# Performance work log

Hardware: AMD Instinct MI355X
Metric: run time of the kernel (lower is better)

## Reference

```python
import jax, jax.numpy as jnp
import numpy as np
import math

DIM = 2048
N_PHASES = 8
B, L = 4, 4096


def setup_inputs() -> dict:
    key = jax.random.key(0)
    ks = jax.random.split(key, 12)
    s = 0.02
    return {
        "x": jax.random.normal(ks[0], (B, L, DIM), dtype=jnp.float32),
        # weights stored [in, out] (transposed vs torch Linear)
        "Wp": jax.random.normal(ks[1], (DIM, N_PHASES), dtype=jnp.float32) * s,
        "bp": jnp.zeros((N_PHASES,), dtype=jnp.float32),
        "Wa": jax.random.normal(ks[2], (DIM, N_PHASES), dtype=jnp.float32) * s,
        "ba": jnp.zeros((N_PHASES,), dtype=jnp.float32),
        "Wv": jax.random.normal(ks[3], (DIM, DIM), dtype=jnp.float32) * s,
        "bv": jnp.zeros((DIM,), dtype=jnp.float32),
        "ln_g": jnp.ones((DIM,), dtype=jnp.float32),
        "ln_b": jnp.zeros((DIM,), dtype=jnp.float32),
        "Wo": jax.random.normal(ks[4], (DIM, DIM), dtype=jnp.float32) * s,
        "bo": jnp.zeros((DIM,), dtype=jnp.float32),
    }


def _layernorm(h, g, b, eps=1e-5):
    mu = jnp.mean(h, axis=-1, keepdims=True)
    var = jnp.var(h, axis=-1, keepdims=True)
    return (h - mu) * jax.lax.rsqrt(var + eps) * g + b


def reference(x, Wp, bp, Wa, ba, Wv, bv, ln_g, ln_b, Wo, bo):
    Llen = x.shape[1]
    phase = jnp.tanh(x @ Wp + bp) * math.pi          # [B,L,P]
    amp = jax.nn.softplus(x @ Wa + ba) + 0.1         # [B,L,P]
    value = x @ Wv + bv                              # [B,L,D]
    # (value[...,None,:] * cos_p[...,None] * amp[...,None]).sum(-2)
    # == value * sum_p(cos_p * amp)  -- algebraic factorization, same math.
    cr = jnp.sum(jnp.cos(phase) * amp, axis=-1, keepdims=True)  # [B,L,1]
    ci = jnp.sum(jnp.sin(phase) * amp, axis=-1, keepdims=True)  # [B,L,1]
    bound = value * (cr + ci)                        # real+imag combined
    retrieved = jnp.cumsum(bound, axis=1)            # [B,L,D]
    h = _layernorm(retrieved / math.sqrt(Llen), ln_g, ln_b)
    return x + h @ Wo + bo
```

## Files before the change

### kernel.cpp

```cpp
#include <hip/hip_runtime.h>

#define DIM   2048
#define LSEQ  4096
#define BATCH 4
#define NTOK  (BATCH*LSEQ)
#define NCH   16
#define CHL   (LSEQ/NCH)
#define PI_F  3.14159265358979f
#define NT    (DIM/64)

typedef __bf16 bf16x8 __attribute__((ext_vector_type(8)));
typedef float  f32x4  __attribute__((ext_vector_type(4)));
typedef float  f32x8  __attribute__((ext_vector_type(8)));
typedef unsigned short ushort4_t __attribute__((ext_vector_type(4)));
typedef unsigned short ushort8 __attribute__((ext_vector_type(8)));

__device__ __forceinline__ unsigned short f2bf(float f) {
    unsigned int u = __float_as_uint(f);
    u += 0x7fffu + ((u >> 16) & 1u);
    return (unsigned short)(u >> 16);
}
__device__ __forceinline__ float bf2f(unsigned short u) {
    return __uint_as_float((unsigned int)u << 16);
}

__device__ __forceinline__ void gload_lds16(const void* g, void* l) {
    __builtin_amdgcn_global_load_lds(
        (const __attribute__((address_space(1))) void*)g,
        (__attribute__((address_space(3))) void*)l, 16, 0, 0);
}

__global__ __launch_bounds__(256) void k_transpose(const float* __restrict__ src,
                                                   unsigned short* __restrict__ dst) {
    __shared__ float tile[32][33];
    int tx = threadIdx.x, ty = threadIdx.y;
    int k0 = blockIdx.y * 32, n0 = blockIdx.x * 32;
#pragma unroll
    for (int r = 0; r < 4; r++)
        tile[ty + r * 8][tx] = src[(size_t)(k0 + ty + r * 8) * DIM + n0 + tx];
    __syncthreads();
#pragma unroll
    for (int r = 0; r < 4; r++)
        dst[(size_t)(n0 + ty + r * 8) * DIM + k0 + tx] = f2bf(tile[tx][ty + r * 8]);
}

__global__ __launch_bounds__(256) void k_prep_wpa(const float* __restrict__ Wp,
                                                  const float* __restrict__ Wa,
                                                  unsigned short* __restrict__ WpaT) {
    int idx = blockIdx.x * 256 + threadIdx.x;
    int p = idx >> 11, k = idx & (DIM - 1);
    float v = (p < 8) ? Wp[(size_t)k * 8 + p] : Wa[(size_t)k * 8 + (p - 8)];
    WpaT[idx] = f2bf(v);
}

__global__ __launch_bounds__(256) void k_sproj_mfma(const float* __restrict__ x,
                                                    const unsigned short* __restrict__ WpaT,
                                                    const float* __restrict__ bp,
                                                    const float* __restrict__ ba,
                                                    float* __restrict__ s,
                                                    unsigned short* __restrict__ xbf) {
    const int t = threadIdx.x;
    const int w = t >> 6, l = t & 63;
    const int r16 = l & 15, q = l >> 4;
    const int rowbase = blockIdx.x * 64 + w * 16;
    const float* xr = x + (size_t)(rowbase + r16) * DIM + q * 8;
    unsigned short* xw = xbf + (size_t)(rowbase + r16) * DIM + q * 8;
    const unsigned short* wrow = WpaT + r16 * DIM + q * 8;

    f32x4 acc = {};
#pragma unroll 8
    for (int ks = 0; ks < 64; ks++) {
        f32x8 xv = *(const f32x8*)(xr + ks * 32);
        ushort8 xo;
#pragma unroll
        for (int j = 0; j < 8; j++) xo[j] = f2bf(xv[j]);
        *(ushort8*)(xw + ks * 32) = xo;
        bf16x8 av = *(const bf16x8*)&xo;
        bf16x8 bv = *(const bf16x8*)(wrow + ks * 32);
        acc = __builtin_amdgcn_mfma_f32_16x16x32_bf16(av, bv, acc, 0, 0, 0);
    }
    const float bpv = bp[r16 & 7], bav = ba[r16 & 7];
#pragma unroll
    for (int j = 0; j < 4; j++) {
        float z = acc[j];
        float zo = __shfl_xor(z, 8);
        float zp = z + bpv, za = zo + bav;
        float ph = tanhf(zp) * PI_F;
        float amp = (za > 20.f ? za : log1pf(expf(za))) + 0.1f;
        float term = (r16 < 8) ? (cosf(ph) + sinf(ph)) * amp : 0.f;
        term += __shfl_xor(term, 1);
        term += __shfl_xor(term, 2);
        term += __shfl_xor(term, 4);
        if (r16 == 0) s[rowbase + q * 4 + j] = term;
    }
}

__device__ __forceinline__ void stage_unit(const unsigned short* __restrict__ src,
                                           unsigned short* dst, int tid) {
    gload_lds16(src,                     dst + tid * 8);
    gload_lds16(src + (size_t)128 * DIM, dst + (tid + 512) * 8);
}

template <int EPI>
__global__ __launch_bounds__(512, 2) void k_gemm256(const unsigned short* __restrict__ A,
                                                    const unsigned short* __restrict__ Bt,
                                                    const float* __restrict__ bias,
                                                    const float* __restrict__ sc,
                                                    const unsigned short* __restrict__ residbf,
                                                    float* __restrict__ C,
                                                    unsigned short* __restrict__ Cbf,
                                                    float* __restrict__ part) {
    __shared__ __align__(16) unsigned short As[2][2][256 * 32];
    __shared__ __align__(16) unsigned short Bs[2][2][256 * 32];
    __shared__ float colsum[2][256];
    const int tid = threadIdx.x;
    const int w = tid >> 6, lane = tid & 63;
    const int wm = w >> 2, wn = w & 3;
    const int r16 = lane & 15, q = lane >> 4;

    int bid = blockIdx.x;
    int wgs = (bid & 7) * 64 + (bid >> 3);
    int tm = wgs >> 3, tn = wgs & 7;
    int brow = tm * 256, bcol = tn * 256;

    const int kq = ((tid & 3) ^ ((tid >> 3) & 3)) * 8;
    const unsigned short* pA = A  + (size_t)(brow + (tid >> 2)) * DIM + kq;
    const unsigned short* pB = Bt + (size_t)(bcol + (tid >> 2)) * DIM + kq;

    const int qs8 = (q ^ ((r16 >> 1) & 3)) * 8;
    const int offA = (wm * 128 + r16) * 32 + qs8;
    const int offB = (wn * 64  + r16) * 32 + qs8;

    f32x4 acc[4][8] = {};

    stage_unit(pA,      &As[0][0][0], tid);
    stage_unit(pB,      &Bs[0][0][0], tid);
    stage_unit(pA + 32, &As[0][1][0], tid);
    stage_unit(pB + 32, &Bs[0][1][0], tid);
    stage_unit(pA + 64, &As[1][0][0], tid);
    asm volatile("s_waitcnt vmcnt(6)" ::: "memory");
    __builtin_amdgcn_s_barrier();

#pragma unroll 2
    for (int t = 0; t < NT; ++t) {
        const int s = t & 1;
        bf16x8 aF[8], bF[4];

#pragma unroll
        for (int i = 0; i < 8; i++) aF[i] = *(const bf16x8*)(&As[s][0][0] + offA + i * 512);
#pragma unroll
        for (int n = 0; n < 4; n++) bF[n] = *(const bf16x8*)(&Bs[s][0][0] + offB + n * 512);
        stage_unit(pB + (t + 1) * 64,      &Bs[s ^ 1][0][0], tid);
        stage_unit(pA + (t + 1) * 64 + 32, &As[s ^ 1][1][0], tid);
        __builtin_amdgcn_s_setprio(1);
#pragma unroll
        for (int n = 0; n < 4; n++)
#pragma unroll
            for (int i = 0; i < 8; i++)
                acc[n][i] = __builtin_amdgcn_mfma_f32_16x16x32_bf16(bF[n], aF[i], acc[n][i], 0, 0, 0);
        __builtin_amdgcn_s_setprio(0);
        asm volatile("s_waitcnt vmcnt(4)" ::: "memory");
        __builtin_amdgcn_s_barrier();

#pragma unroll
        for (int i = 0; i < 8; i++) aF[i] = *(const bf16x8*)(&As[s][1][0] + offA + i * 512);
#pragma unroll
        for (int n = 0; n < 4; n++) bF[n] = *(const bf16x8*)(&Bs[s][1][0] + offB + n * 512);
        stage_unit(pB + (t + 1) * 64 + 32, &Bs[s ^ 1][1][0], tid);
        stage_unit(pA + (t + 2) * 64,      &As[s][0][0], tid);
        __builtin_amdgcn_s_setprio(1);
#pragma unroll
        for (int n = 0; n < 4; n++)
#pragma unroll
            for (int i = 0; i < 8; i++)
                acc[n][i] = __builtin_amdgcn_mfma_f32_16x16x32_bf16(bF[n], aF[i], acc[n][i], 0, 0, 0);
        __builtin_amdgcn_s_setprio(0);
        asm volatile("s_waitcnt vmcnt(4)" ::: "memory");
        __builtin_amdgcn_s_barrier();
    }
    asm volatile("s_waitcnt vmcnt(0)" ::: "memory");

    float cs[4][4] = {};
#pragma unroll
    for (int nf = 0; nf < 4; nf++) {
        const int c0 = bcol + wn * 64 + nf * 16 + q * 4;
        const f32x4 b4 = *(const f32x4*)(bias + c0);
#pragma unroll
        for (int mi = 0; mi < 8; mi++) {
            const int r = brow + wm * 128 + mi * 16 + r16;
            if (EPI == 0) {
                const float scr = sc[r];
                ushort4_t o;
#pragma unroll
                for (int j = 0; j < 4; j++) {
                    float v = (acc[nf][mi][j] + b4[j]) * scr;
                    cs[nf][j] += v;
                    o[j] = f2bf(v);
                }
                *(ushort4_t*)(Cbf + (size_t)r * DIM + c0) = o;
            } else {
                ushort4_t rsd = *(const ushort4_t*)(residbf + (size_t)r * DIM + c0);
                f32x4 v;
#pragma unroll
                for (int j = 0; j < 4; j++) v[j] = acc[nf][mi][j] + b4[j] + bf2f(rsd[j]);
                *(f32x4*)(C + (size_t)r * DIM + c0) = v;
            }
        }
    }
    if (EPI == 0) {
#pragma unroll
        for (int nf = 0; nf < 4; nf++)
#pragma unroll
            for (int j = 0; j < 4; j++) {
                float v = cs[nf][j];
                v += __shfl_xor(v, 1);
                v += __shfl_xor(v, 2);
                v += __shfl_xor(v, 4);
                v += __shfl_xor(v, 8);
                cs[nf][j] = v;
            }
        if (r16 == 0) {
#pragma unroll
            for (int nf = 0; nf < 4; nf++) {
                f32x4 o;
#pragma unroll
                for (int j = 0; j < 4; j++) o[j] = cs[nf][j];
                *(f32x4*)(&colsum[wm][wn * 64 + nf * 16 + q * 4]) = o;
            }
        }
        __syncthreads();
        if (tid < 256)
            part[(size_t)(brow >> 8) * DIM + bcol + tid] = colsum[0][tid] + colsum[1][tid];
    }
}

__global__ __launch_bounds__(256) void k_scan_offsets(float* __restrict__ part) {
    int tid = blockIdx.x * 256 + threadIdx.x;
    int d = tid & (DIM - 1);
    int b = tid >> 11;
    float run = 0.f;
    for (int ch = 0; ch < NCH; ch++) {
        size_t idx = ((size_t)b * NCH + ch) * DIM + d;
        float v = part[idx];
        part[idx] = run;
        run += v;
    }
}

__global__ __launch_bounds__(256) void k_scan_apply(const unsigned short* __restrict__ boundbf,
                                                    const float* __restrict__ part,
                                                    float* __restrict__ ret) {
    int tid = blockIdx.x * 256 + threadIdx.x;
    int d = tid & (DIM - 1);
    int ch = (tid >> 11) & (NCH - 1);
    int b = tid >> 15;
    float run = part[tid];
    size_t base = ((size_t)b * LSEQ + (size_t)ch * CHL) * DIM + d;
    const unsigned short* p = boundbf + base;
    float* o = ret + base;
    for (int i = 0; i < CHL; i++) {
        run += bf2f(p[(size_t)i * DIM]);
        o[(size_t)i * DIM] = run;
    }
}

__global__ __launch_bounds__(256) void k_lnorm(const float* __restrict__ ret,
                                               const float* __restrict__ g,
                                               const float* __restrict__ bta,
                                               unsigned short* __restrict__ h) {
    int row = blockIdx.x, t = threadIdx.x;
    const float4* r4 = (const float4*)(ret + (size_t)row * DIM);
    float4 v0 = r4[2 * t], v1 = r4[2 * t + 1];
    const float scl = 1.0f / 64.0f;
    v0.x *= scl; v0.y *= scl; v0.z *= scl; v0.w *= scl;
    v1.x *= scl; v1.y *= scl; v1.z *= scl; v1.w *= scl;
    float sum = v0.x + v0.y + v0.z + v0.w + v1.x + v1.y + v1.z + v1.w;
    float ss  = v0.x*v0.x + v0.y*v0.y + v0.z*v0.z + v0.w*v0.w
              + v1.x*v1.x + v1.y*v1.y + v1.z*v1.z + v1.w*v1.w;
#pragma unroll
    for (int off = 32; off; off >>= 1) { sum += __shfl_down(sum, off); ss += __shfl_down(ss, off); }
    __shared__ float red[4][2];
    __shared__ float mu_s, rstd_s;
    int w = t >> 6, lane = t & 63;
    if (lane == 0) { red[w][0] = sum; red[w][1] = ss; }
    __syncthreads();
    if (t == 0) {
        float S = red[0][0] + red[1][0] + red[2][0] + red[3][0];
        float Q = red[0][1] + red[1][1] + red[2][1] + red[3][1];
        float mu = S / DIM;
        float var = Q / DIM - mu * mu;
        mu_s = mu; rstd_s = rsqrtf(var + 1e-5f);
    }
    __syncthreads();
    float mu = mu_s, rstd = rstd_s;
    f32x8 gv = *(const f32x8*)(g + t * 8);
    f32x8 bv = *(const f32x8*)(bta + t * 8);
    float vv[8] = { v0.x, v0.y, v0.z, v0.w, v1.x, v1.y, v1.z, v1.w };
    ushort8 o;
#pragma unroll
    for (int j = 0; j < 8; j++) o[j] = f2bf((vv[j] - mu) * rstd * gv[j] + bv[j]);
    *(ushort8*)(h + (size_t)row * DIM + t * 8) = o;
}

extern "C" void kernel_launch(void* const* d_in, const int* in_sizes, int n_in,
                              void* d_out, int out_size, void* d_ws, size_t ws_size,
                              hipStream_t stream) {
    const float* x   = (const float*)d_in[0];
    const float* Wp  = (const float*)d_in[1];
    const float* bp  = (const float*)d_in[2];
    const float* Wa  = (const float*)d_in[3];
    const float* ba  = (const float*)d_in[4];
    const float* Wv  = (const float*)d_in[5];
    const float* bv  = (const float*)d_in[6];
    const float* lng = (const float*)d_in[7];
    const float* lnb = (const float*)d_in[8];
    const float* Wo  = (const float*)d_in[9];
    const float* bo  = (const float*)d_in[10];
    float* out = (float*)d_out;

    char* ws = (char*)d_ws;
    unsigned short* x_bf  = (unsigned short*)ws; ws += (size_t)NTOK * DIM * 2;
    unsigned short* h_bf  = (unsigned short*)ws; ws += (size_t)NTOK * DIM * 2;
    unsigned short* WvT   = (unsigned short*)ws; ws += (size_t)DIM * DIM * 2;
    unsigned short* WoT   = (unsigned short*)ws; ws += (size_t)DIM * DIM * 2;
    unsigned short* WpaT  = (unsigned short*)ws; ws += (size_t)16 * DIM * 2;
    float* svec           = (float*)ws;          ws += (size_t)NTOK * 4;
    unsigned short* bound = (unsigned short*)ws; ws += (size_t)NTOK * DIM * 2;
    float* part           = (float*)ws;          ws += (size_t)BATCH * NCH * DIM * 4;
    float* ret            = out;

    dim3 tb(32, 8);
    k_transpose<<<dim3(64, 64), tb, 0, stream>>>(Wv, WvT);
    k_transpose<<<dim3(64, 64), tb, 0, stream>>>(Wo, WoT);
    k_prep_wpa<<<128, 256, 0, stream>>>(Wp, Wa, WpaT);
    k_sproj_mfma<<<NTOK / 64, 256, 0, stream>>>(x, WpaT, bp, ba, svec, x_bf);

    k_gemm256<0><<<512, 512, 0, stream>>>(x_bf, WvT, bv, svec, nullptr, nullptr, bound, part);

    k_scan_offsets<<<BATCH * DIM / 256, 256, 0, stream>>>(part);
    k_scan_apply<<<BATCH * NCH * DIM / 256, 256, 0, stream>>>(bound, part, ret);

    k_lnorm<<<NTOK, 256, 0, stream>>>(ret, lng, lnb, h_bf);

    k_gemm256<1><<<512, 512, 0, stream>>>(h_bf, WoT, bo, nullptr, x_bf, out, nullptr, nullptr);
}
```

Measured before the change: 477.5 us.

## Split GEMM k-step into four quarter phases with finer-grained barrier interleaving

Each half k-step of the GEMM main loop is split into two phases of four A fragments each, so every iteration has four LDS-read / global-stage / MFMA phases instead of two. Each phase issues one staging load and is surrounded by extra barriers. The row mapping of the accumulators and the epilogue index are changed to match. The aim is lower register pressure (half the A fragments live at once) and tighter interleaving of loads with MFMA, at the cost of more barriers and dropping the unroll-2 pragma.

```diff
diff --git a/kernel.cpp b/kernel.cpp
--- a/kernel.cpp
+++ b/kernel.cpp
@@ -141,41 +141,75 @@
     asm volatile("s_waitcnt vmcnt(6)" ::: "memory");
     __builtin_amdgcn_s_barrier();
 
-#pragma unroll 2
     for (int t = 0; t < NT; ++t) {
         const int s = t & 1;
-        bf16x8 aF[8], bF[4];
-
-#pragma unroll
-        for (int i = 0; i < 8; i++) aF[i] = *(const bf16x8*)(&As[s][0][0] + offA + i * 512);
-#pragma unroll
-        for (int n = 0; n < 4; n++) bF[n] = *(const bf16x8*)(&Bs[s][0][0] + offB + n * 512);
-        stage_unit(pB + (t + 1) * 64,      &Bs[s ^ 1][0][0], tid);
-        stage_unit(pA + (t + 1) * 64 + 32, &As[s ^ 1][1][0], tid);
+        unsigned short* A0 = &As[s][0][0];
+        unsigned short* A1 = &As[s][1][0];
+        unsigned short* B0 = &Bs[s][0][0];
+        unsigned short* B1 = &Bs[s][1][0];
+        unsigned short* nA1 = &As[s ^ 1][1][0];
+        unsigned short* nB0 = &Bs[s ^ 1][0][0];
+        unsigned short* nB1 = &Bs[s ^ 1][1][0];
+        const unsigned short* pAn = pA + (t + 1) * 64;
+        const unsigned short* pBn = pB + (t + 1) * 64;
+
+        bf16x8 aF[4], bF[4];
+#pragma unroll
+        for (int i = 0; i < 4; i++) aF[i] = *(const bf16x8*)(A0 + offA + i * 512);
+#pragma unroll
+        for (int i = 0; i < 4; i++) bF[i] = *(const bf16x8*)(B0 + offB + i * 512);
+        stage_unit(pBn, nB0, tid);
+        __builtin_amdgcn_s_barrier();
         __builtin_amdgcn_s_setprio(1);
 #pragma unroll
         for (int n = 0; n < 4; n++)
 #pragma unroll
-            for (int i = 0; i < 8; i++)
+            for (int i = 0; i < 4; i++)
                 acc[n][i] = __builtin_amdgcn_mfma_f32_16x16x32_bf16(bF[n], aF[i], acc[n][i], 0, 0, 0);
         __builtin_amdgcn_s_setprio(0);
-        asm volatile("s_waitcnt vmcnt(4)" ::: "memory");
-        __builtin_amdgcn_s_barrier();
-
-#pragma unroll
-        for (int i = 0; i < 8; i++) aF[i] = *(const bf16x8*)(&As[s][1][0] + offA + i * 512);
-#pragma unroll
-        for (int n = 0; n < 4; n++) bF[n] = *(const bf16x8*)(&Bs[s][1][0] + offB + n * 512);
-        stage_unit(pB + (t + 1) * 64 + 32, &Bs[s ^ 1][1][0], tid);
-        stage_unit(pA + (t + 2) * 64,      &As[s][0][0], tid);
+        __builtin_amdgcn_s_barrier();
+
+#pragma unroll
+        for (int i = 0; i < 4; i++) aF[i] = *(const bf16x8*)(A0 + offA + 2048 + i * 512);
+        stage_unit(pAn + 32, nA1, tid);
+        __builtin_amdgcn_s_barrier();
         __builtin_amdgcn_s_setprio(1);
 #pragma unroll
         for (int n = 0; n < 4; n++)
 #pragma unroll
-            for (int i = 0; i < 8; i++)
+            for (int i = 0; i < 4; i++)
+                acc[n][4 + i] = __builtin_amdgcn_mfma_f32_16x16x32_bf16(bF[n], aF[i], acc[n][4 + i], 0, 0, 0);
+        __builtin_amdgcn_s_setprio(0);
+        asm volatile("s_waitcnt vmcnt(6)" ::: "memory");
+        __builtin_amdgcn_s_barrier();
+
+#pragma unroll
+        for (int i = 0; i < 4; i++) aF[i] = *(const bf16x8*)(A1 + offA + i * 512);
+#pragma unroll
+        for (int i = 0; i < 4; i++) bF[i] = *(const bf16x8*)(B1 + offB + i * 512);
+        stage_unit(pBn + 32, nB1, tid);
+        __builtin_amdgcn_s_barrier();
+        __builtin_amdgcn_s_setprio(1);
+#pragma unroll
+        for (int n = 0; n < 4; n++)
+#pragma unroll
+            for (int i = 0; i < 4; i++)
                 acc[n][i] = __builtin_amdgcn_mfma_f32_16x16x32_bf16(bF[n], aF[i], acc[n][i], 0, 0, 0);
         __builtin_amdgcn_s_setprio(0);
-        asm volatile("s_waitcnt vmcnt(4)" ::: "memory");
+        __builtin_amdgcn_s_barrier();
+
+#pragma unroll
+        for (int i = 0; i < 4; i++) aF[i] = *(const bf16x8*)(A1 + offA + 2048 + i * 512);
+        stage_unit(pA + (t + 2) * 64, A0, tid);
+        __builtin_amdgcn_s_barrier();
+        __builtin_amdgcn_s_setprio(1);
+#pragma unroll
+        for (int n = 0; n < 4; n++)
+#pragma unroll
+            for (int i = 0; i < 4; i++)
+                acc[n][4 + i] = __builtin_amdgcn_mfma_f32_16x16x32_bf16(bF[n], aF[i], acc[n][4 + i], 0, 0, 0);
+        __builtin_amdgcn_s_setprio(0);
+        asm volatile("s_waitcnt vmcnt(6)" ::: "memory");
         __builtin_amdgcn_s_barrier();
     }
     asm volatile("s_waitcnt vmcnt(0)" ::: "memory");
@@ -186,14 +220,14 @@
         const int c0 = bcol + wn * 64 + nf * 16 + q * 4;
         const f32x4 b4 = *(const f32x4*)(bias + c0);
 #pragma unroll
-        for (int mi = 0; mi < 8; mi++) {
-            const int r = brow + wm * 128 + mi * 16 + r16;
+        for (int ci = 0; ci < 8; ci++) {
+            const int r = brow + wm * 128 + ((ci >> 2) << 6) + ((ci & 3) << 4) + r16;
             if (EPI == 0) {
                 const float scr = sc[r];
                 ushort4_t o;
 #pragma unroll
                 for (int j = 0; j < 4; j++) {
-                    float v = (acc[nf][mi][j] + b4[j]) * scr;
+                    float v = (acc[nf][ci][j] + b4[j]) * scr;
                     cs[nf][j] += v;
                     o[j] = f2bf(v);
                 }
@@ -202,7 +236,7 @@
                 ushort4_t rsd = *(const ushort4_t*)(residbf + (size_t)r * DIM + c0);
                 f32x4 v;
 #pragma unroll
-                for (int j = 0; j < 4; j++) v[j] = acc[nf][mi][j] + b4[j] + bf2f(rsd[j]);
+                for (int j = 0; j < 4; j++) v[j] = acc[nf][ci][j] + b4[j] + bf2f(rsd[j]);
                 *(f32x4*)(C + (size_t)r * DIM + c0) = v;
             }
         }
```

Result: faster. 461.1 us (-3.4%).
